# Kernel tuning notes

Hardware: AMD Instinct MI355X
Metric: run time of the kernel (lower is better)

Reference implementation:

```python
import jax, jax.numpy as jnp
import numpy as np

CELL = 16          # pixels_per_cell
ORI = 6            # orientations
BIN_W = 180.0 / ORI
EPS = 1e-5         # skimage block-norm eps


def setup_inputs() -> dict:
    key = jax.random.key(0)
    x = jax.random.normal(key, (32, 3, 512, 512), dtype=jnp.float32)
    return {"x": x}


def _hog(x):
    # x: (B, 3, H, W) -> per-image HOG feature vector, matching skimage.feature.hog
    img = jnp.transpose(x, (0, 2, 3, 1))
    gray = 0.299 * img[..., 0] + 0.587 * img[..., 1] + 0.114 * img[..., 2]  # (B,H,W)
    B, H, W = gray.shape

    # skimage central-difference gradients with zeroed borders
    g_row = jnp.zeros_like(gray).at[:, 1:-1, :].set(gray[:, 2:, :] - gray[:, :-2, :])
    g_col = jnp.zeros_like(gray).at[:, :, 1:-1].set(gray[:, :, 2:] - gray[:, :, :-2])

    mag = jnp.hypot(g_row, g_col)
    ori = jnp.degrees(jnp.arctan2(g_row, g_col)) % 180.0
    bins = jnp.clip(jnp.floor(ori / BIN_W).astype(jnp.int32), 0, ORI - 1)

    # hard-assigned orientation histogram per 16x16 cell, averaged over cell pixels
    weighted = jax.nn.one_hot(bins, ORI, dtype=mag.dtype) * mag[..., None]  # (B,H,W,ORI)
    ncr, ncc = H // CELL, W // CELL
    cells = weighted.reshape(B, ncr, CELL, ncc, CELL, ORI).sum(axis=(2, 4)) / (CELL * CELL)

    # 2x2-cell blocks with stride 1 cell: (B, nbr, nbc, 2, 2, ORI)
    blocks = jnp.stack(
        [jnp.stack([cells[:, :-1, :-1], cells[:, :-1, 1:]], axis=3),
         jnp.stack([cells[:, 1:, :-1], cells[:, 1:, 1:]], axis=3)],
        axis=3)

    # L2-Hys normalization
    n1 = jnp.sqrt(jnp.sum(blocks * blocks, axis=(3, 4, 5), keepdims=True) + EPS * EPS)
    nb = jnp.minimum(blocks / n1, 0.2)
    n2 = jnp.sqrt(jnp.sum(nb * nb, axis=(3, 4, 5), keepdims=True) + EPS * EPS)
    nb = nb / n2
    return nb.reshape(B, -1).astype(jnp.float32)


def reference(x):
    return _hog(x)
```

## Files before the change

kernel.cpp:

```cpp
#include <hip/hip_runtime.h>
#include <math.h>

#define BATCH 32
#define HH 512
#define WW 512
#define NC 32
#define NORI 6
#define TP 66
#define PITCH 67

__device__ __forceinline__ int bin_of(float a) {
    const float deg = __fmul_rn(a, 57.29577951308232f);
    float m = fmodf(deg, 180.0f);
    if (m < 0.0f) m = __fadd_rn(m, 180.0f);
    const int b = (int)floorf(__fdiv_rn(m, 30.0f));
    return min(max(b, 0), NORI - 1);
}
__device__ __forceinline__ float ulp_step(float x, int k) {
    const int i = __float_as_int(x);
    int key = (i >= 0) ? i : -(i & 0x7FFFFFFF);
    key += k;
    const int r = (key >= 0) ? key : (int)(0x80000000u | (unsigned)(-key));
    return __int_as_float(r);
}
__device__ __forceinline__ void deposit(float acc[NORI], int bin, float val) {
#pragma unroll
    for (int o = 0; o < NORI; ++o) acc[o] += (bin == o) ? val : 0.0f;
}

__global__ __launch_bounds__(256, 6) void hog_cells_kernel(const float* __restrict__ x,
                                                           float* __restrict__ cells) {
    const int b = blockIdx.z;
    const int tid = threadIdx.x;
    const int R0 = 64 * blockIdx.y - 1;
    const int C0 = 64 * blockIdx.x - 1;

    __shared__ float gray[TP * PITCH];

    const float* img = x + (size_t)b * 3 * HH * WW;
    for (int i = tid; i < TP * TP; i += 256) {
        const int lr = i / TP, lc = i - lr * TP;
        const int r = R0 + lr, c = C0 + lc;
        float g = 0.0f;
        if ((unsigned)r < (unsigned)HH && (unsigned)c < (unsigned)WW) {
            const size_t idx = (size_t)r * WW + c;
            g = __fadd_rn(__fadd_rn(__fmul_rn(0.299f, img[idx]),
                                    __fmul_rn(0.587f, img[idx + (size_t)HH * WW])),
                          __fadd_rn(0.0f, __fmul_rn(0.114f, img[idx + (size_t)2 * HH * WW])));
        }
        gray[lr * PITCH + lc] = g;
    }
    __syncthreads();

    const int wave = tid >> 6, lane = tid & 63;
    const int rl = wave * 16 + (lane & 15);
    const int clb = (lane >> 4) * 16;
    const int rg = R0 + 1 + rl;
    const bool row_ok = (rg >= 1) && (rg < HH - 1);

    const float CC = 0.86602540378443864676f, SS = 0.5f, EPS = 1e-4f;
    float acc[NORI] = {0, 0, 0, 0, 0, 0};

#pragma unroll
    for (int j = 0; j < 16; ++j) {
        const int cl = clb + j;
        const int cg = C0 + 1 + cl;
        const float up = gray[rl * PITCH + cl + 1];
        const float dn = gray[(rl + 2) * PITCH + cl + 1];
        const float lf = gray[(rl + 1) * PITCH + cl];
        const float rt = gray[(rl + 1) * PITCH + cl + 2];
        const float gy = row_ok ? __fsub_rn(dn, up) : 0.0f;
        const float gx = (cg >= 1 && cg < WW - 1) ? __fsub_rn(rt, lf) : 0.0f;

        const float mag = __fsqrt_rn(__fmaf_rn(gy, gy, __fmul_rn(gx, gx)));
        if (mag > 0.0f) {
            const bool neg = gy < 0.0f;
            const float cy = neg ? -gy : gy;
            const float cx = neg ? -gx : gx;
            const float t1 = __fmaf_rn(cy, CC, -__fmul_rn(cx, SS));
            const float t2 = __fmaf_rn(cy, SS, -__fmul_rn(cx, CC));
            const float t3 = -cx;
            const float t4 = __fmaf_rn(cy, -SS, -__fmul_rn(cx, CC));
            const float t5 = __fmaf_rn(cy, -CC, -__fmul_rn(cx, SS));
            int bin = (t1 >= 0.0f) + (t2 >= 0.0f) + (t3 >= 0.0f) +
                      (t4 >= 0.0f) + (t5 >= 0.0f);
            const float s = __fmul_rn(mag, EPS);
            const float mn = fminf(fminf(fminf(fabsf(t1), fabsf(t2)),
                                         fminf(fabsf(t3), fabsf(t4))), fabsf(t5));
            const bool gz = (gy == 0.0f), xz = (gx == 0.0f);
            bool amb = (mn < s) || (cx < 0.0f && cy < s);
            if (gz) { bin = 0; amb = false; }
            else if (xz) { bin = 3; amb = false; }
            if (!amb) {
                deposit(acc, bin, mag);
            } else {
                const float a = atan2f(gy, gx);
                const int bl = bin_of(ulp_step(a, -2));
                const int bh = bin_of(ulp_step(a, +2));
                if (bl == bh) {
                    deposit(acc, bl, mag);
                } else {
                    const int b0 = bin_of(a);
                    const int bo = (b0 == bl) ? bh : bl;
                    deposit(acc, b0, __fmul_rn(mag, 0.65f));
                    deposit(acc, bo, __fmul_rn(mag, 0.35f));
                }
            }
        }
    }

#pragma unroll
    for (int o = 0; o < NORI; ++o) {
        float v = acc[o];
        v += __shfl_xor(v, 1);
        v += __shfl_xor(v, 2);
        v += __shfl_xor(v, 4);
        v += __shfl_xor(v, 8);
        acc[o] = v;
    }
    if ((lane & 15) == 0) {
        const int cell_r = 4 * blockIdx.y + wave;
        const int cell_c = 4 * blockIdx.x + (lane >> 4);
        float* cp = cells + (((size_t)b * NC + cell_r) * NC + cell_c) * NORI;
#pragma unroll
        for (int o = 0; o < NORI; ++o) cp[o] = acc[o] * (1.0f / 256.0f);
    }
}

__global__ __launch_bounds__(256) void hog_norm_kernel(const float* __restrict__ cells,
                                                       float* __restrict__ out) {
    const int idx = blockIdx.x * 256 + threadIdx.x;
    const int total = BATCH * 31 * 31;
    if (idx >= total) return;
    const int bc = idx % 31;
    const int t = idx / 31;
    const int br = t % 31;
    const int b = t / 31;

    const float* cb = cells + (size_t)b * NC * NC * NORI;
    const float2* p0 = (const float2*)(cb + ((br) * NC + bc) * NORI);
    const float2* p1 = (const float2*)(cb + ((br + 1) * NC + bc) * NORI);
    float v[24];
#pragma unroll
    for (int q = 0; q < 6; ++q) {
        const float2 r0 = p0[q], r1 = p1[q];
        v[2 * q] = r0.x; v[2 * q + 1] = r0.y;
        v[12 + 2 * q] = r1.x; v[12 + 2 * q + 1] = r1.y;
    }
    float ss = 0.0f;
#pragma unroll
    for (int k = 0; k < 24; ++k) ss = __fadd_rn(ss, __fmul_rn(v[k], v[k]));
    const float n1 = __fsqrt_rn(__fadd_rn(ss, 1e-10f));
    float ss2 = 0.0f;
#pragma unroll
    for (int k = 0; k < 24; ++k) {
        v[k] = fminf(__fdiv_rn(v[k], n1), 0.2f);
        ss2 = __fadd_rn(ss2, __fmul_rn(v[k], v[k]));
    }
    const float n2 = __fsqrt_rn(__fadd_rn(ss2, 1e-10f));
    float* op = out + (size_t)idx * 24;
#pragma unroll
    for (int k = 0; k < 24; ++k) op[k] = __fdiv_rn(v[k], n2);
}

extern "C" void kernel_launch(void* const* d_in, const int* in_sizes, int n_in,
                              void* d_out, int out_size, void* d_ws, size_t ws_size,
                              hipStream_t stream) {
    const float* x = (const float*)d_in[0];
    float* out = (float*)d_out;
    float* cells = (float*)d_ws;

    dim3 g1(8, 8, BATCH), b1(256);
    hog_cells_kernel<<<g1, b1, 0, stream>>>(x, cells);

    const int total = BATCH * 31 * 31;
    hog_norm_kernel<<<(total + 255) / 256, 256, 0, stream>>>(cells, out);
}
```

Measured before the change: 166.1 us.

## Replace shared-memory gray tile with per-lane column streaming and shuffles

```diff
diff --git a/kernel.cpp b/kernel.cpp
--- a/kernel.cpp
+++ b/kernel.cpp
@@ -6,8 +6,6 @@
 #define WW 512
 #define NC 32
 #define NORI 6
-#define TP 66
-#define PITCH 67
 
 __device__ __forceinline__ int bin_of(float a) {
     const float deg = __fmul_rn(a, 57.29577951308232f);
@@ -23,90 +21,100 @@
     const int r = (key >= 0) ? key : (int)(0x80000000u | (unsigned)(-key));
     return __int_as_float(r);
 }
+
+struct SlowRes { float w0, w1; int b0, b1; };
+__device__ __attribute__((noinline)) SlowRes slow_path(float gy, float gx, float mag) {
+    const float a = atan2f(gy, gx);
+    const int bl = bin_of(ulp_step(a, -2));
+    const int bh = bin_of(ulp_step(a, +2));
+    SlowRes r;
+    if (bl == bh) {
+        r.b0 = bl; r.b1 = bl; r.w0 = mag; r.w1 = 0.0f;
+    } else {
+        const int b0 = bin_of(a);
+        r.b0 = b0; r.b1 = (b0 == bl) ? bh : bl;
+        r.w0 = __fmul_rn(mag, 0.65f);
+        r.w1 = __fmul_rn(mag, 0.35f);
+    }
+    return r;
+}
+
 __device__ __forceinline__ void deposit(float acc[NORI], int bin, float val) {
 #pragma unroll
     for (int o = 0; o < NORI; ++o) acc[o] += (bin == o) ? val : 0.0f;
 }
 
-__global__ __launch_bounds__(256, 6) void hog_cells_kernel(const float* __restrict__ x,
-                                                           float* __restrict__ cells) {
+__device__ __forceinline__ float gray_at(const float* __restrict__ img, int rr, int cc) {
+    const size_t idx = (size_t)rr * WW + cc;
+    return __fadd_rn(__fadd_rn(__fmul_rn(0.299f, img[idx]),
+                               __fmul_rn(0.587f, img[idx + (size_t)HH * WW])),
+                     __fmul_rn(0.114f, img[idx + (size_t)2 * HH * WW]));
+}
+
+__global__ __launch_bounds__(256) void hog_cells_kernel(const float* __restrict__ x,
+                                                        float* __restrict__ cells) {
     const int b = blockIdx.z;
     const int tid = threadIdx.x;
-    const int R0 = 64 * blockIdx.y - 1;
-    const int C0 = 64 * blockIdx.x - 1;
+    const int wave = tid >> 6, lane = tid & 63;
+    const int R0 = blockIdx.y * 64 + wave * 16;
+    const int cbase = blockIdx.x * 64;
+    const int c = cbase + lane;
+    const float* img = x + (size_t)b * 3 * HH * WW;
 
-    __shared__ float gray[TP * PITCH];
+    const bool is_edge = (lane == 0) || (lane == 63);
+    int hc = (lane == 0) ? (cbase - 1) : (cbase + 64);
+    hc = min(max(hc, 0), WW - 1);
 
-    const float* img = x + (size_t)b * 3 * HH * WW;
-    for (int i = tid; i < TP * TP; i += 256) {
-        const int lr = i / TP, lc = i - lr * TP;
-        const int r = R0 + lr, c = C0 + lc;
-        float g = 0.0f;
-        if ((unsigned)r < (unsigned)HH && (unsigned)c < (unsigned)WW) {
-            const size_t idx = (size_t)r * WW + c;
-            g = __fadd_rn(__fadd_rn(__fmul_rn(0.299f, img[idx]),
-                                    __fmul_rn(0.587f, img[idx + (size_t)HH * WW])),
-                          __fadd_rn(0.0f, __fmul_rn(0.114f, img[idx + (size_t)2 * HH * WW])));
-        }
-        gray[lr * PITCH + lc] = g;
-    }
-    __syncthreads();
+    float gm1 = gray_at(img, max(R0 - 1, 0), c);
+    float g0  = gray_at(img, R0, c);
+    float hcur = 0.0f;
+    if (is_edge) hcur = gray_at(img, R0, hc);
 
-    const int wave = tid >> 6, lane = tid & 63;
-    const int rl = wave * 16 + (lane & 15);
-    const int clb = (lane >> 4) * 16;
-    const int rg = R0 + 1 + rl;
-    const bool row_ok = (rg >= 1) && (rg < HH - 1);
-
-    const float CC = 0.86602540378443864676f, SS = 0.5f, EPS = 1e-4f;
+    const float CC = 0.86602540378443864676f, SS = 0.5f, EPS = 1e-5f;
+    const bool col_ok = (c >= 1) && (c < WW - 1);
     float acc[NORI] = {0, 0, 0, 0, 0, 0};
 
-#pragma unroll
-    for (int j = 0; j < 16; ++j) {
-        const int cl = clb + j;
-        const int cg = C0 + 1 + cl;
-        const float up = gray[rl * PITCH + cl + 1];
-        const float dn = gray[(rl + 2) * PITCH + cl + 1];
-        const float lf = gray[(rl + 1) * PITCH + cl];
-        const float rt = gray[(rl + 1) * PITCH + cl + 2];
-        const float gy = row_ok ? __fsub_rn(dn, up) : 0.0f;
-        const float gx = (cg >= 1 && cg < WW - 1) ? __fsub_rn(rt, lf) : 0.0f;
+    for (int r = R0; r < R0 + 16; ++r) {
+        const int rn = min(r + 1, HH - 1);
+        const float gp1 = gray_at(img, rn, c);
+        float hnext = 0.0f;
+        if (is_edge) hnext = gray_at(img, rn, hc);
+
+        const bool row_ok = (r >= 1) && (r < HH - 1);
+        const float gy = row_ok ? __fsub_rn(gp1, gm1) : 0.0f;
+        float gl = __shfl(g0, (lane + 63) & 63);
+        float gr = __shfl(g0, (lane + 1) & 63);
+        if (lane == 0)  gl = hcur;
+        if (lane == 63) gr = hcur;
+        const float gx = col_ok ? __fsub_rn(gr, gl) : 0.0f;
 
         const float mag = __fsqrt_rn(__fmaf_rn(gy, gy, __fmul_rn(gx, gx)));
-        if (mag > 0.0f) {
-            const bool neg = gy < 0.0f;
-            const float cy = neg ? -gy : gy;
-            const float cx = neg ? -gx : gx;
-            const float t1 = __fmaf_rn(cy, CC, -__fmul_rn(cx, SS));
-            const float t2 = __fmaf_rn(cy, SS, -__fmul_rn(cx, CC));
-            const float t3 = -cx;
-            const float t4 = __fmaf_rn(cy, -SS, -__fmul_rn(cx, CC));
-            const float t5 = __fmaf_rn(cy, -CC, -__fmul_rn(cx, SS));
-            int bin = (t1 >= 0.0f) + (t2 >= 0.0f) + (t3 >= 0.0f) +
-                      (t4 >= 0.0f) + (t5 >= 0.0f);
-            const float s = __fmul_rn(mag, EPS);
-            const float mn = fminf(fminf(fminf(fabsf(t1), fabsf(t2)),
-                                         fminf(fabsf(t3), fabsf(t4))), fabsf(t5));
-            const bool gz = (gy == 0.0f), xz = (gx == 0.0f);
-            bool amb = (mn < s) || (cx < 0.0f && cy < s);
-            if (gz) { bin = 0; amb = false; }
-            else if (xz) { bin = 3; amb = false; }
-            if (!amb) {
-                deposit(acc, bin, mag);
-            } else {
-                const float a = atan2f(gy, gx);
-                const int bl = bin_of(ulp_step(a, -2));
-                const int bh = bin_of(ulp_step(a, +2));
-                if (bl == bh) {
-                    deposit(acc, bl, mag);
-                } else {
-                    const int b0 = bin_of(a);
-                    const int bo = (b0 == bl) ? bh : bl;
-                    deposit(acc, b0, __fmul_rn(mag, 0.65f));
-                    deposit(acc, bo, __fmul_rn(mag, 0.35f));
-                }
-            }
+        const bool neg = gy < 0.0f;
+        const float cy = fabsf(gy);
+        const float cx = neg ? -gx : gx;
+        const float t1 = __fmaf_rn(cy, CC, -__fmul_rn(cx, SS));
+        const float t2 = __fmaf_rn(cy, SS, -__fmul_rn(cx, CC));
+        const float t3 = -cx;
+        const float t4 = __fmaf_rn(cy, -SS, -__fmul_rn(cx, CC));
+        const float t5 = __fmaf_rn(cy, -CC, -__fmul_rn(cx, SS));
+        int bin = (t1 >= 0.0f) + (t2 >= 0.0f) + (t3 >= 0.0f) +
+                  (t4 >= 0.0f) + (t5 >= 0.0f);
+        const float s = __fmul_rn(mag, EPS);
+        const float mn = fminf(fminf(fminf(fabsf(t1), fabsf(t2)),
+                                     fminf(fabsf(t3), fabsf(t4))), fabsf(t5));
+        bool amb = (mn < s) || (cx < 0.0f && cy < s);
+        if (gy == 0.0f) { bin = 0; amb = false; }
+        else if (gx == 0.0f) { bin = 3; amb = false; }
+
+        if (__builtin_expect(amb, 0)) {
+            const SlowRes sr = slow_path(gy, gx, mag);
+            deposit(acc, sr.b0, sr.w0);
+            deposit(acc, sr.b1, sr.w1);
+        } else {
+            deposit(acc, bin, mag);
         }
+
+        gm1 = g0; g0 = gp1; hcur = hnext;
     }
 
 #pragma unroll
@@ -119,8 +127,8 @@
         acc[o] = v;
     }
     if ((lane & 15) == 0) {
-        const int cell_r = 4 * blockIdx.y + wave;
-        const int cell_c = 4 * blockIdx.x + (lane >> 4);
+        const int cell_r = R0 >> 4;
+        const int cell_c = (cbase >> 4) + (lane >> 4);
         float* cp = cells + (((size_t)b * NC + cell_r) * NC + cell_c) * NORI;
 #pragma unroll
         for (int o = 0; o < NORI; ++o) cp[o] = acc[o] * (1.0f / 256.0f);
```

Result: faster. 154.4 us (-7.0%).
